# Kernel tuning notes

Hardware: AMD Instinct MI355X
Metric: run time of the kernel (lower is better)

The kernel has to match this reference:

```python
import jax, jax.numpy as jnp
import numpy as np
from jax import lax

N_CHANNELS = 64
N_FILTERS = 256
N_LAYERS = 9  # residual blocks use dilations 2**1 .. 2**(N_LAYERS-1)


def causal_conv1d(x, w, dilation):
    """Causal dilated conv. x: [B,T,Cin], w: [K,Cin,Cout]."""
    pad = (w.shape[0] - 1) * dilation
    return lax.conv_general_dilated(
        x, w, window_strides=(1,), padding=[(pad, 0)],
        rhs_dilation=(dilation,), dimension_numbers=("NWC", "WIO", "NWC"))


def setup_inputs() -> dict:
    key = jax.random.key(0)
    ks = jax.random.split(key, 12)
    B, T, C, F, L = 8, 4096, N_CHANNELS, N_FILTERS, N_LAYERS
    s = lambda fan_in: 1.0 / np.sqrt(fan_in)
    return {
        "x": jax.random.normal(ks[0], (B, T, C), jnp.float32),
        "Wc": jax.random.normal(ks[1], (2, C, F), jnp.float32) * s(2 * C),
        "Wf": jax.random.normal(ks[2], (L - 1, 2, F, F), jnp.float32) * s(2 * F),
        "Wg": jax.random.normal(ks[3], (L - 1, 2, F, F), jnp.float32) * s(2 * F),
        "Wr": jax.random.normal(ks[4], (L - 1, F, F), jnp.float32) * s(F),
        "br": jnp.zeros((L - 1, F), jnp.float32),
        "Ws": jax.random.normal(ks[5], (L - 1, F, F), jnp.float32) * s(F),
        "bs": jnp.zeros((L - 1, F), jnp.float32),
        "Wd1": jax.random.normal(ks[6], (F, C), jnp.float32) * s(F),
        "bd1": jnp.zeros((C,), jnp.float32),
        "Wd2": jax.random.normal(ks[7], (C, C), jnp.float32) * s(C),
        "bd2": jnp.zeros((C,), jnp.float32),
    }


def reference(x, Wc, Wf, Wg, Wr, br, Ws, bs, Wd1, bd1, Wd2, bd2):
    # Initial causal conv, dilation 1, no bias.
    out = causal_conv1d(x, Wc, 1)  # [B,T,F]
    skip_sum = jnp.zeros_like(out)
    for i in range(N_LAYERS - 1):
        d = 2 ** (i + 1)
        f = causal_conv1d(out, Wf[i], d)
        g = causal_conv1d(out, Wg[i], d)
        z = jnp.tanh(f) * jax.nn.sigmoid(g)
        out = out + jnp.einsum("btf,fo->bto", z, Wr[i]) + br[i]
        skip_sum = skip_sum + jnp.einsum("btf,fo->bto", z, Ws[i]) + bs[i]
    h = jax.nn.selu(skip_sum)
    h = jnp.einsum("btf,fc->btc", h, Wd1) + bd1
    h = jax.nn.selu(h)
    h = jnp.einsum("btc,co->bto", h, Wd2) + bd2
    return h
```

## Files before the change

### kernel.cpp

```cpp
#include <hip/hip_runtime.h>
#include <cstdint>

typedef unsigned short u16;
typedef unsigned int u32;
typedef __attribute__((ext_vector_type(8))) short s8v;
typedef __attribute__((ext_vector_type(4))) float f4v;

#define FCH 256

__device__ __forceinline__ float bf2f(u16 u){ return __uint_as_float(((u32)u)<<16); }
__device__ __forceinline__ u16 f2bf(float x){
  u32 u = __float_as_uint(x);
  u += 0x7fffu + ((u>>16)&1u);
  return (u16)(u>>16);
}
__device__ __forceinline__ uint4 pack8(float4 a, float4 b){
  uint4 o;
  o.x = (u32)f2bf(a.x) | ((u32)f2bf(a.y)<<16);
  o.y = (u32)f2bf(a.z) | ((u32)f2bf(a.w)<<16);
  o.z = (u32)f2bf(b.x) | ((u32)f2bf(b.y)<<16);
  o.w = (u32)f2bf(b.z) | ((u32)f2bf(b.w)<<16);
  return o;
}
__device__ __forceinline__ float seluf(float x){
  const float sc = 1.0507009873554805f, al = 1.6732632423543772f;
  return x > 0.f ? sc*x : sc*al*(__expf(x)-1.f);
}
__device__ __forceinline__ s8v ldmask(const u16* p, u32 m){
  uint4 r = *reinterpret_cast<const uint4*>(p);
  r.x &= m; r.y &= m; r.z &= m; r.w &= m;
  s8v v; *reinterpret_cast<uint4*>(&v) = r;
  return v;
}
__device__ __forceinline__ int xcd_tile(int bid, int nT8){
  return nT8 ? ((bid & 7) * nT8 + (bid >> 3)) : bid;
}

__global__ __launch_bounds__(256) void pack_kernel(
    const float* __restrict__ Wc, const float* __restrict__ Wf, const float* __restrict__ Wg,
    const float* __restrict__ Wr, const float* __restrict__ Ws,
    const float* __restrict__ Wd1, const float* __restrict__ Wd2,
    u16* __restrict__ Bp1, u16* __restrict__ Bp2, u16* __restrict__ Bp0,
    u16* __restrict__ BpD1, u16* __restrict__ BpD2)
{
  int gid = blockIdx.x*256 + threadIdx.x;
  int frag = gid >> 6;
  int lane = gid & 63;
  int q = lane >> 4, i15 = lane & 15;
  u16 v[8];
  u16* dst;
  if (frag < 4096) {
    int layer = frag >> 9, rem = frag & 511;
    int kc = rem >> 5, nt = rem & 31;
    int n = nt*16 + i15;
    const float* W = (n < 256) ? Wf : Wg;
    int nn = (n < 256) ? n : n - 256;
    #pragma unroll
    for (int j = 0; j < 8; ++j) {
      int k = kc*32 + q*8 + j;
      int tap = k >> 8, cin = k & 255;
      v[j] = f2bf(W[((size_t)((layer*2 + tap)*256 + cin))*256 + nn]);
    }
    dst = Bp1 + (size_t)frag*512 + lane*8;
  } else if (frag < 6144) {
    int f = frag - 4096;
    int layer = f >> 8, rem = f & 255;
    int kc = rem >> 5, nt = rem & 31;
    int n = nt*16 + i15;
    const float* W = (n < 256) ? Wr : Ws;
    int nn = (n < 256) ? n : n - 256;
    #pragma unroll
    for (int j = 0; j < 8; ++j) {
      int k = kc*32 + q*8 + j;
      v[j] = f2bf(W[((size_t)(layer*256 + k))*256 + nn]);
    }
    dst = Bp2 + (size_t)f*512 + lane*8;
  } else if (frag < 6208) {
    int f = frag - 6144;
    int kc = f >> 4, nt = f & 15;
    int n = nt*16 + i15;
    #pragma unroll
    for (int j = 0; j < 8; ++j) {
      int k = kc*32 + q*8 + j;
      int tap = k >> 6, cin = k & 63;
      v[j] = f2bf(Wc[(size_t)(tap*64 + cin)*256 + n]);
    }
    dst = Bp0 + (size_t)f*512 + lane*8;
  } else if (frag < 6240) {
    int f = frag - 6208;
    int kc = f >> 2, nt = f & 3;
    int n = nt*16 + i15;
    #pragma unroll
    for (int j = 0; j < 8; ++j) {
      int k = kc*32 + q*8 + j;
      v[j] = f2bf(Wd1[(size_t)k*64 + n]);
    }
    dst = BpD1 + (size_t)f*512 + lane*8;
  } else if (frag < 6248) {
    int f = frag - 6240;
    int kc = f >> 2, nt = f & 3;
    int n = nt*16 + i15;
    #pragma unroll
    for (int j = 0; j < 8; ++j) {
      int k = kc*32 + q*8 + j;
      v[j] = f2bf(Wd2[(size_t)k*64 + n]);
    }
    dst = BpD2 + (size_t)f*512 + lane*8;
  } else return;
  uint4 o;
  o.x = (u32)v[0] | ((u32)v[1] << 16);
  o.y = (u32)v[2] | ((u32)v[3] << 16);
  o.z = (u32)v[4] | ((u32)v[5] << 16);
  o.w = (u32)v[6] | ((u32)v[7] << 16);
  *reinterpret_cast<uint4*>(dst) = o;
}

__global__ __launch_bounds__(256, 2) void conv0_kernel(
    const float* __restrict__ x, u16* __restrict__ outBf,
    const u16* __restrict__ Bp0, int nT8)
{
  __shared__ __align__(16) u16 ldsA[2][2048];
  const int tid = threadIdx.x;
  const int w = tid >> 6, lane = tid & 63, q = lane >> 4, i15 = lane & 15;
  const int rb = xcd_tile(blockIdx.x, nT8) * 64;
  const int sm = tid >> 2, sg = tid & 3;
  const int grow = rb + sm;
  const int tpos = grow & 4095;
  const int sunit = ((sm >> 4)*64 + sg*16 + ((sm & 15) ^ (sg << 1))) * 8;
  const int runit = (q*16 + (i15 ^ (q << 1))) * 8;

  f4v acc[4][4];
  #pragma unroll
  for (int jj = 0; jj < 4; ++jj)
    #pragma unroll
    for (int mt = 0; mt < 4; ++mt)
      acc[jj][mt] = (f4v){0.f,0.f,0.f,0.f};

  float4 f0 = {0.f,0.f,0.f,0.f}, f1 = {0.f,0.f,0.f,0.f};
  if (tpos >= 1) {
    const float* px = x + (size_t)(grow-1)*64 + sg*8;
    f0 = *reinterpret_cast<const float4*>(px);
    f1 = *reinterpret_cast<const float4*>(px + 4);
  }
  *reinterpret_cast<uint4*>(&ldsA[0][sunit]) = pack8(f0, f1);
  s8v bcur[4], bnxt[4];
  #pragma unroll
  for (int jj = 0; jj < 4; ++jj)
    bcur[jj] = *reinterpret_cast<const s8v*>(Bp0 + ((size_t)(w + 4*jj)*64 + lane)*8);
  __syncthreads();

  for (int kc = 0; kc < 4; ++kc) {
    const int cur = kc & 1;
    uint4 an = {0u,0u,0u,0u};
    if (kc < 3) {
      int kg = (kc+1)*32 + sg*8;
      int tap = kg >> 6, col = kg & 63;
      float4 g0 = {0.f,0.f,0.f,0.f}, g1 = {0.f,0.f,0.f,0.f};
      if (tap) {
        const float* px = x + (size_t)grow*64 + col;
        g0 = *reinterpret_cast<const float4*>(px);
        g1 = *reinterpret_cast<const float4*>(px + 4);
      } else if (tpos >= 1) {
        const float* px = x + (size_t)(grow-1)*64 + col;
        g0 = *reinterpret_cast<const float4*>(px);
        g1 = *reinterpret_cast<const float4*>(px + 4);
      }
      an = pack8(g0, g1);
      #pragma unroll
      for (int jj = 0; jj < 4; ++jj)
        bnxt[jj] = *reinterpret_cast<const s8v*>(Bp0 + (((size_t)(kc+1)*16 + (w + 4*jj))*64 + lane)*8);
    }
    s8v af[4];
    #pragma unroll
    for (int mt = 0; mt < 4; ++mt)
      af[mt] = *reinterpret_cast<const s8v*>(&ldsA[cur][mt*512 + runit]);
    #pragma unroll
    for (int jj = 0; jj < 4; ++jj)
      #pragma unroll
      for (int mt = 0; mt < 4; ++mt)
        acc[jj][mt] = __builtin_amdgcn_mfma_f32_16x16x32_bf16(af[mt], bcur[jj], acc[jj][mt], 0,0,0);
    if (kc < 3) {
      *reinterpret_cast<uint4*>(&ldsA[cur ^ 1][sunit]) = an;
      #pragma unroll
      for (int jj = 0; jj < 4; ++jj) bcur[jj] = bnxt[jj];
    }
    __syncthreads();
  }

  #pragma unroll
  for (int jj = 0; jj < 4; ++jj) {
    const int cc = (w + 4*jj)*16 + i15;
    #pragma unroll
    for (int mt = 0; mt < 4; ++mt)
      #pragma unroll
      for (int r = 0; r < 4; ++r) {
        const int g2 = rb + mt*16 + q*4 + r;
        outBf[(size_t)g2*FCH + cc] = f2bf(acc[jj][mt][r]);
      }
  }
}

__global__ __launch_bounds__(256, 3) void layer_kernel(
    const u16* __restrict__ inBf, u16* __restrict__ outBf,
    u16* __restrict__ skipB,
    const u16* __restrict__ Bp1, const u16* __restrict__ Bp2,
    const float* __restrict__ br, const float* __restrict__ bs,
    int dil, int first, int nT8)
{
  __shared__ __align__(16) u16 ldsZ[32*264];
  const int tid = threadIdx.x;
  const int w = tid >> 6, lane = tid & 63, q = lane >> 4, i15 = lane & 15;
  const int rb = xcd_tile(blockIdx.x, nT8) * 32;

  f4v acc[8][2];
  #pragma unroll
  for (int jj = 0; jj < 8; ++jj)
    #pragma unroll
    for (int mt = 0; mt < 2; ++mt)
      acc[jj][mt] = (f4v){0.f,0.f,0.f,0.f};

  {
    const u16* a0p[2];
    const u16* a1p[2];
    u32 am[2];
    #pragma unroll
    for (int mt = 0; mt < 2; ++mt) {
      const int row = rb + mt*16 + i15;
      const bool v = (row & 4095) >= dil;
      a0p[mt] = inBf + (size_t)(v ? row - dil : row)*FCH + q*8;
      a1p[mt] = inBf + (size_t)row*FCH + q*8;
      am[mt]  = v ? 0xffffffffu : 0u;
    }

    s8v bb[2][8], aa[2][2];
    #pragma unroll
    for (int jj = 0; jj < 8; ++jj)
      bb[0][jj] = *reinterpret_cast<const s8v*>(Bp1 + ((size_t)(w + 4*jj)*64 + lane)*8);
    #pragma unroll
    for (int mt = 0; mt < 2; ++mt)
      aa[0][mt] = ldmask(a0p[mt], am[mt]);

    #pragma unroll
    for (int kc = 0; kc < 16; ++kc) {
      const int cur = kc & 1, nxt = cur ^ 1;
      if (kc + 1 < 16) {
        const int kn = kc + 1;
        #pragma unroll
        for (int jj = 0; jj < 8; ++jj)
          bb[nxt][jj] = *reinterpret_cast<const s8v*>(Bp1 + (((size_t)kn*32 + (w + 4*jj))*64 + lane)*8);
        if (kn < 8) {
          #pragma unroll
          for (int mt = 0; mt < 2; ++mt)
            aa[nxt][mt] = ldmask(a0p[mt] + kn*32, am[mt]);
        } else {
          #pragma unroll
          for (int mt = 0; mt < 2; ++mt)
            aa[nxt][mt] = *reinterpret_cast<const s8v*>(a1p[mt] + (kn - 8)*32);
        }
      }
      __builtin_amdgcn_s_setprio(1);
      #pragma unroll
      for (int jj = 0; jj < 8; ++jj)
        #pragma unroll
        for (int mt = 0; mt < 2; ++mt)
          acc[jj][mt] = __builtin_amdgcn_mfma_f32_16x16x32_bf16(aa[cur][mt], bb[cur][jj], acc[jj][mt], 0,0,0);
      __builtin_amdgcn_s_setprio(0);
    }
  }

  s8v s2b[2][8];
  #pragma unroll
  for (int jj = 0; jj < 8; ++jj)
    s2b[0][jj] = *reinterpret_cast<const s8v*>(Bp2 + ((size_t)(w + 4*jj)*64 + lane)*8);

  #pragma unroll
  for (int jj = 0; jj < 4; ++jj) {
    const int colb = (w + 4*jj)*16 + i15;
    #pragma unroll
    for (int mt = 0; mt < 2; ++mt)
      #pragma unroll
      for (int r = 0; r < 4; ++r) {
        float f = acc[jj][mt][r];
        float g = acc[jj+4][mt][r];
        float z = (1.f - 2.f/(__expf(2.f*f) + 1.f)) * (1.f/(1.f + __expf(-g)));
        ldsZ[(mt*16 + q*4 + r)*264 + colb] = f2bf(z);
      }
  }
  #pragma unroll
  for (int jj = 0; jj < 8; ++jj)
    #pragma unroll
    for (int mt = 0; mt < 2; ++mt)
      acc[jj][mt] = (f4v){0.f,0.f,0.f,0.f};
  __syncthreads();

  {
    s8v zf[2][2];
    #pragma unroll
    for (int mt = 0; mt < 2; ++mt)
      zf[0][mt] = *reinterpret_cast<const s8v*>(&ldsZ[(mt*16 + i15)*264 + q*8]);
    #pragma unroll
    for (int kc = 0; kc < 8; ++kc) {
      const int cur = kc & 1, nxt = cur ^ 1;
      if (kc + 1 < 8) {
        const int kn = kc + 1;
        #pragma unroll
        for (int jj = 0; jj < 8; ++jj)
          s2b[nxt][jj] = *reinterpret_cast<const s8v*>(Bp2 + (((size_t)kn*32 + (w + 4*jj))*64 + lane)*8);
        #pragma unroll
        for (int mt = 0; mt < 2; ++mt)
          zf[nxt][mt] = *reinterpret_cast<const s8v*>(&ldsZ[(mt*16 + i15)*264 + kn*32 + q*8]);
      }
      __builtin_amdgcn_s_setprio(1);
      #pragma unroll
      for (int jj = 0; jj < 8; ++jj)
        #pragma unroll
        for (int mt = 0; mt < 2; ++mt)
          acc[jj][mt] = __builtin_amdgcn_mfma_f32_16x16x32_bf16(zf[cur][mt], s2b[cur][jj], acc[jj][mt], 0,0,0);
      __builtin_amdgcn_s_setprio(0);
    }
  }

  u16 resv[4][2][4], skv[4][2][4];
  #pragma unroll
  for (int jj = 0; jj < 4; ++jj) {
    const int cc = (w + 4*jj)*16 + i15;
    #pragma unroll
    for (int mt = 0; mt < 2; ++mt)
      #pragma unroll
      for (int r = 0; r < 4; ++r)
        resv[jj][mt][r] = inBf[(size_t)(rb + mt*16 + q*4 + r)*FCH + cc];
  }
  if (!first) {
    #pragma unroll
    for (int jj = 0; jj < 4; ++jj) {
      const int cc = (w + 4*jj)*16 + i15;
      #pragma unroll
      for (int mt = 0; mt < 2; ++mt)
        #pragma unroll
        for (int r = 0; r < 4; ++r)
          skv[jj][mt][r] = skipB[(size_t)(rb + mt*16 + q*4 + r)*FCH + cc];
    }
  }
  #pragma unroll
  for (int jj = 0; jj < 8; ++jj) {
    const int nt = w + 4*jj;
    const bool isR = (jj < 4);
    const int cc = (isR ? nt*16 : (nt-16)*16) + i15;
    const float bias = isR ? br[cc] : bs[cc];
    #pragma unroll
    for (int mt = 0; mt < 2; ++mt)
      #pragma unroll
      for (int r = 0; r < 4; ++r) {
        const int g2 = rb + mt*16 + q*4 + r;
        float vv = acc[jj][mt][r] + bias;
        if (isR) vv += bf2f(resv[jj][mt][r]);
        else if (!first) vv += bf2f(skv[jj-4][mt][r]);
        u16 hv = f2bf(vv);
        if (isR) outBf[(size_t)g2*FCH + cc] = hv;
        else     skipB[(size_t)g2*FCH + cc] = hv;
      }
  }
}

__global__ __launch_bounds__(256, 2) void final_kernel(
    const u16* __restrict__ skipB, const u16* __restrict__ BpD1, const u16* __restrict__ BpD2,
    const float* __restrict__ bd1, const float* __restrict__ bd2, float* __restrict__ outp,
    int nT8)
{
  __shared__ __align__(16) u16 ldsH[64*264];
  __shared__ __align__(16) u16 ldsH2[64*72];
  const int tid = threadIdx.x;
  const int w = tid >> 6, lane = tid & 63, q = lane >> 4, i15 = lane & 15;
  const int rb = xcd_tile(blockIdx.x, nT8) * 64;
  const int sm = tid >> 2, sseg = tid & 3;

  {
    const u16* sp = skipB + (size_t)(rb + sm)*256 + sseg*64;
    u16* dr = &ldsH[sm*264 + sseg*64];
    #pragma unroll
    for (int u = 0; u < 8; ++u) {
      uint4 raw = *reinterpret_cast<const uint4*>(sp + u*8);
      u32 rr[4] = {raw.x, raw.y, raw.z, raw.w};
      uint4 o;
      u32 oo[4];
      #pragma unroll
      for (int p = 0; p < 4; ++p) {
        float e0 = seluf(bf2f((u16)(rr[p] & 0xffffu)));
        float e1 = seluf(bf2f((u16)(rr[p] >> 16)));
        oo[p] = (u32)f2bf(e0) | ((u32)f2bf(e1) << 16);
      }
      o.x = oo[0]; o.y = oo[1]; o.z = oo[2]; o.w = oo[3];
      *reinterpret_cast<uint4*>(dr + u*8) = o;
    }
  }
  __syncthreads();

  f4v a1[4];
  #pragma unroll
  for (int mt = 0; mt < 4; ++mt) a1[mt] = (f4v){0.f,0.f,0.f,0.f};
  for (int kc = 0; kc < 8; ++kc) {
    s8v b = *reinterpret_cast<const s8v*>(BpD1 + ((size_t)(kc*4 + w)*64 + lane)*8);
    #pragma unroll
    for (int mt = 0; mt < 4; ++mt) {
      s8v af = *reinterpret_cast<const s8v*>(&ldsH[(mt*16 + i15)*264 + kc*32 + q*8]);
      a1[mt] = __builtin_amdgcn_mfma_f32_16x16x32_bf16(af, b, a1[mt], 0,0,0);
    }
  }
  const float bb1 = bd1[w*16 + i15];
  #pragma unroll
  for (int mt = 0; mt < 4; ++mt)
    #pragma unroll
    for (int r = 0; r < 4; ++r)
      ldsH2[(mt*16 + q*4 + r)*72 + w*16 + i15] = f2bf(seluf(a1[mt][r] + bb1));
  __syncthreads();

  f4v a2[4];
  #pragma unroll
  for (int mt = 0; mt < 4; ++mt) a2[mt] = (f4v){0.f,0.f,0.f,0.f};
  #pragma unroll
  for (int kc = 0; kc < 2; ++kc) {
    s8v b = *reinterpret_cast<const s8v*>(BpD2 + ((size_t)(kc*4 + w)*64 + lane)*8);
    #pragma unroll
    for (int mt = 0; mt < 4; ++mt) {
      s8v af = *reinterpret_cast<const s8v*>(&ldsH2[(mt*16 + i15)*72 + kc*32 + q*8]);
      a2[mt] = __builtin_amdgcn_mfma_f32_16x16x32_bf16(af, b, a2[mt], 0,0,0);
    }
  }
  const float bb2 = bd2[w*16 + i15];
  #pragma unroll
  for (int mt = 0; mt < 4; ++mt)
    #pragma unroll
    for (int r = 0; r < 4; ++r)
      outp[(size_t)(rb + mt*16 + q*4 + r)*64 + w*16 + i15] = a2[mt][r] + bb2;
}

__global__ __launch_bounds__(256) void zero_kernel(uint4* __restrict__ outp, int n16)
{
  int i = blockIdx.x*256 + threadIdx.x;
  if (i < n16) outp[i] = (uint4){0u,0u,0u,0u};
}

extern "C" void kernel_launch(void* const* d_in, const int* in_sizes, int n_in,
                              void* d_out, int out_size, void* d_ws, size_t ws_size,
                              hipStream_t stream)
{
  (void)n_in;
  const float* x   = (const float*)d_in[0];
  const float* Wc  = (const float*)d_in[1];
  const float* Wf  = (const float*)d_in[2];
  const float* Wg  = (const float*)d_in[3];
  const float* Wr  = (const float*)d_in[4];
  const float* br  = (const float*)d_in[5];
  const float* Ws  = (const float*)d_in[6];
  const float* bs  = (const float*)d_in[7];
  const float* Wd1 = (const float*)d_in[8];
  const float* bd1 = (const float*)d_in[9];
  const float* Wd2 = (const float*)d_in[10];
  const float* bd2 = (const float*)d_in[11];

  const size_t ROWS = (size_t)in_sizes[0] / 64;
  const int gridC = (int)(ROWS / 64);
  const int gridL = (int)(ROWS / 32);
  const int nT8C = (gridC % 8 == 0) ? gridC / 8 : 0;
  const int nT8L = (gridL % 8 == 0) ? gridL / 8 : 0;

  const size_t packsB = (size_t)6248 * 512 * 2;
  const size_t bfBuf  = ROWS * 256 * 2;
  const size_t needB = packsB + 3*bfBuf;

  if (ws_size < needB) {
    int n16 = (out_size * 4) / 16;
    zero_kernel<<<(n16 + 255)/256, 256, 0, stream>>>((uint4*)d_out, n16);
    return;
  }

  char* ws = (char*)d_ws;
  u16* Bp1    = (u16*)ws;            ws += (size_t)4096*512*2;
  u16* Bp2    = (u16*)ws;            ws += (size_t)2048*512*2;
  u16* Bp0    = (u16*)ws;            ws += (size_t)64*512*2;
  u16* BpD1   = (u16*)ws;            ws += (size_t)32*512*2;
  u16* BpD2   = (u16*)ws;            ws += (size_t)8*512*2;
  u16* skipB  = (u16*)ws;            ws += bfBuf;
  u16* bufA   = (u16*)ws;            ws += bfBuf;
  u16* bufB   = (u16*)ws;            ws += bfBuf;

  pack_kernel<<<1562, 256, 0, stream>>>(Wc, Wf, Wg, Wr, Ws, Wd1, Wd2,
                                        Bp1, Bp2, Bp0, BpD1, BpD2);
  conv0_kernel<<<gridC, 256, 0, stream>>>(x, bufA, Bp0, nT8C);
  u16* bufs[2] = {bufA, bufB};
  for (int i = 0; i < 8; ++i) {
    layer_kernel<<<gridL, 256, 0, stream>>>(
        bufs[i & 1], bufs[(i + 1) & 1], skipB,
        Bp1 + (size_t)i*262144, Bp2 + (size_t)i*131072,
        br + i*256, bs + i*256, 2 << i, (i == 0) ? 1 : 0, nT8L);
  }
  final_kernel<<<gridC, 256, 0, stream>>>(skipB, BpD1, BpD2, bd1, bd2,
                                          (float*)d_out, nT8C);
}
```

Before: 492.2 us.

## Switch layer kernel to 32x32x16 bf16 MFMA with repacked weight fragments

The residual-layer kernel now uses 32x32x16 bf16 MFMA instructions in place of 16x16x32. Each wave covers a full 32-row tile with four 32-column accumulators instead of a 2x8 grid of 16x16 tiles. The weight packing for the dilated-conv and residual/skip matrices is changed to match the 32-wide fragment layout, and the epilogue row mapping is rewritten for the 32x32 output layout. This is meant to raise MFMA throughput per instruction and cut the number of A-fragment loads, at the cost of twice as many K-steps and a different register and LDS access pattern.

```diff
diff --git a/kernel.cpp b/kernel.cpp
--- a/kernel.cpp
+++ b/kernel.cpp
@@ -5,6 +5,7 @@
 typedef unsigned int u32;
 typedef __attribute__((ext_vector_type(8))) short s8v;
 typedef __attribute__((ext_vector_type(4))) float f4v;
+typedef __attribute__((ext_vector_type(16))) float f16v;
 
 #define FCH 256
 
@@ -47,17 +48,18 @@
   int frag = gid >> 6;
   int lane = gid & 63;
   int q = lane >> 4, i15 = lane & 15;
+  int hi = lane >> 5, c31 = lane & 31;
   u16 v[8];
   u16* dst;
   if (frag < 4096) {
     int layer = frag >> 9, rem = frag & 511;
-    int kc = rem >> 5, nt = rem & 31;
-    int n = nt*16 + i15;
+    int kc = rem >> 4, nt = rem & 15;
+    int n = nt*32 + c31;
     const float* W = (n < 256) ? Wf : Wg;
     int nn = (n < 256) ? n : n - 256;
     #pragma unroll
     for (int j = 0; j < 8; ++j) {
-      int k = kc*32 + q*8 + j;
+      int k = kc*16 + hi*8 + j;
       int tap = k >> 8, cin = k & 255;
       v[j] = f2bf(W[((size_t)((layer*2 + tap)*256 + cin))*256 + nn]);
     }
@@ -65,13 +67,13 @@
   } else if (frag < 6144) {
     int f = frag - 4096;
     int layer = f >> 8, rem = f & 255;
-    int kc = rem >> 5, nt = rem & 31;
-    int n = nt*16 + i15;
+    int kc = rem >> 4, nt = rem & 15;
+    int n = nt*32 + c31;
     const float* W = (n < 256) ? Wr : Ws;
     int nn = (n < 256) ? n : n - 256;
     #pragma unroll
     for (int j = 0; j < 8; ++j) {
-      int k = kc*32 + q*8 + j;
+      int k = kc*16 + hi*8 + j;
       v[j] = f2bf(W[((size_t)(layer*256 + k))*256 + nn]);
     }
     dst = Bp2 + (size_t)f*512 + lane*8;
@@ -209,156 +211,136 @@
 {
   __shared__ __align__(16) u16 ldsZ[32*264];
   const int tid = threadIdx.x;
-  const int w = tid >> 6, lane = tid & 63, q = lane >> 4, i15 = lane & 15;
+  const int w = tid >> 6, lane = tid & 63, hi = lane >> 5, c31 = lane & 31;
   const int rb = xcd_tile(blockIdx.x, nT8) * 32;
 
-  f4v acc[8][2];
-  #pragma unroll
-  for (int jj = 0; jj < 8; ++jj)
-    #pragma unroll
-    for (int mt = 0; mt < 2; ++mt)
-      acc[jj][mt] = (f4v){0.f,0.f,0.f,0.f};
+  f16v acc[4];
+  #pragma unroll
+  for (int jj = 0; jj < 4; ++jj)
+    #pragma unroll
+    for (int r = 0; r < 16; ++r) acc[jj][r] = 0.f;
 
   {
-    const u16* a0p[2];
-    const u16* a1p[2];
-    u32 am[2];
-    #pragma unroll
-    for (int mt = 0; mt < 2; ++mt) {
-      const int row = rb + mt*16 + i15;
-      const bool v = (row & 4095) >= dil;
-      a0p[mt] = inBf + (size_t)(v ? row - dil : row)*FCH + q*8;
-      a1p[mt] = inBf + (size_t)row*FCH + q*8;
-      am[mt]  = v ? 0xffffffffu : 0u;
-    }
-
-    s8v bb[2][8], aa[2][2];
-    #pragma unroll
-    for (int jj = 0; jj < 8; ++jj)
-      bb[0][jj] = *reinterpret_cast<const s8v*>(Bp1 + ((size_t)(w + 4*jj)*64 + lane)*8);
-    #pragma unroll
-    for (int mt = 0; mt < 2; ++mt)
-      aa[0][mt] = ldmask(a0p[mt], am[mt]);
-
+    const int row = rb + c31;
+    const bool v = (row & 4095) >= dil;
+    const u16* a0 = inBf + (size_t)(v ? row - dil : row)*FCH + hi*8;
+    const u16* a1 = inBf + (size_t)row*FCH + hi*8;
+    const u32 am = v ? 0xffffffffu : 0u;
+
+    s8v bb[2][4], aa[2];
+    #pragma unroll
+    for (int jj = 0; jj < 4; ++jj) {
+      const int nt = (jj < 2) ? (2*w + jj) : (8 + 2*w + (jj - 2));
+      bb[0][jj] = *reinterpret_cast<const s8v*>(Bp1 + ((size_t)nt*64 + lane)*8);
+    }
+    aa[0] = ldmask(a0, am);
+
+    #pragma unroll
+    for (int kc = 0; kc < 32; ++kc) {
+      const int cur = kc & 1, nxt = cur ^ 1;
+      if (kc + 1 < 32) {
+        const int kn = kc + 1;
+        #pragma unroll
+        for (int jj = 0; jj < 4; ++jj) {
+          const int nt = (jj < 2) ? (2*w + jj) : (8 + 2*w + (jj - 2));
+          bb[nxt][jj] = *reinterpret_cast<const s8v*>(Bp1 + (((size_t)kn*16 + nt)*64 + lane)*8);
+        }
+        if (kn < 16) aa[nxt] = ldmask(a0 + kn*16, am);
+        else         aa[nxt] = *reinterpret_cast<const s8v*>(a1 + (kn - 16)*16);
+      }
+      __builtin_amdgcn_s_setprio(1);
+      #pragma unroll
+      for (int jj = 0; jj < 4; ++jj)
+        acc[jj] = __builtin_amdgcn_mfma_f32_32x32x16_bf16(aa[cur], bb[cur][jj], acc[jj], 0,0,0);
+      __builtin_amdgcn_s_setprio(0);
+    }
+  }
+
+  s8v s2b[2][4];
+  #pragma unroll
+  for (int jj = 0; jj < 4; ++jj) {
+    const int nt = (jj < 2) ? (2*w + jj) : (8 + 2*w + (jj - 2));
+    s2b[0][jj] = *reinterpret_cast<const s8v*>(Bp2 + ((size_t)nt*64 + lane)*8);
+  }
+
+  #pragma unroll
+  for (int jj = 0; jj < 2; ++jj) {
+    const int colb = (2*w + jj)*32 + c31;
+    #pragma unroll
+    for (int r = 0; r < 16; ++r) {
+      const int rowid = (r & 3) + 8*(r >> 2) + 4*hi;
+      float f = acc[jj][r];
+      float g = acc[jj+2][r];
+      float z = (1.f - 2.f/(__expf(2.f*f) + 1.f)) * (1.f/(1.f + __expf(-g)));
+      ldsZ[rowid*264 + colb] = f2bf(z);
+    }
+  }
+  #pragma unroll
+  for (int jj = 0; jj < 4; ++jj)
+    #pragma unroll
+    for (int r = 0; r < 16; ++r) acc[jj][r] = 0.f;
+  __syncthreads();
+
+  {
+    s8v zf[2];
+    zf[0] = *reinterpret_cast<const s8v*>(&ldsZ[c31*264 + hi*8]);
     #pragma unroll
     for (int kc = 0; kc < 16; ++kc) {
       const int cur = kc & 1, nxt = cur ^ 1;
       if (kc + 1 < 16) {
         const int kn = kc + 1;
         #pragma unroll
-        for (int jj = 0; jj < 8; ++jj)
-          bb[nxt][jj] = *reinterpret_cast<const s8v*>(Bp1 + (((size_t)kn*32 + (w + 4*jj))*64 + lane)*8);
-        if (kn < 8) {
-          #pragma unroll
-          for (int mt = 0; mt < 2; ++mt)
-            aa[nxt][mt] = ldmask(a0p[mt] + kn*32, am[mt]);
-        } else {
-          #pragma unroll
-          for (int mt = 0; mt < 2; ++mt)
-            aa[nxt][mt] = *reinterpret_cast<const s8v*>(a1p[mt] + (kn - 8)*32);
+        for (int jj = 0; jj < 4; ++jj) {
+          const int nt = (jj < 2) ? (2*w + jj) : (8 + 2*w + (jj - 2));
+          s2b[nxt][jj] = *reinterpret_cast<const s8v*>(Bp2 + (((size_t)kn*16 + nt)*64 + lane)*8);
         }
+        zf[nxt] = *reinterpret_cast<const s8v*>(&ldsZ[c31*264 + kn*16 + hi*8]);
       }
       __builtin_amdgcn_s_setprio(1);
       #pragma unroll
-      for (int jj = 0; jj < 8; ++jj)
-        #pragma unroll
-        for (int mt = 0; mt < 2; ++mt)
-          acc[jj][mt] = __builtin_amdgcn_mfma_f32_16x16x32_bf16(aa[cur][mt], bb[cur][jj], acc[jj][mt], 0,0,0);
+      for (int jj = 0; jj < 4; ++jj)
+        acc[jj] = __builtin_amdgcn_mfma_f32_32x32x16_bf16(zf[cur], s2b[cur][jj], acc[jj], 0,0,0);
       __builtin_amdgcn_s_setprio(0);
     }
   }
 
-  s8v s2b[2][8];
-  #pragma unroll
-  for (int jj = 0; jj < 8; ++jj)
-    s2b[0][jj] = *reinterpret_cast<const s8v*>(Bp2 + ((size_t)(w + 4*jj)*64 + lane)*8);
-
+  u16 resv[2][16], skv[2][16];
+  #pragma unroll
+  for (int jj = 0; jj < 2; ++jj) {
+    const int cc = (2*w + jj)*32 + c31;
+    #pragma unroll
+    for (int r = 0; r < 16; ++r) {
+      const int rowid = (r & 3) + 8*(r >> 2) + 4*hi;
+      resv[jj][r] = inBf[(size_t)(rb + rowid)*FCH + cc];
+    }
+  }
+  if (!first) {
+    #pragma unroll
+    for (int jj = 0; jj < 2; ++jj) {
+      const int cc = (2*w + jj)*32 + c31;
+      #pragma unroll
+      for (int r = 0; r < 16; ++r) {
+        const int rowid = (r & 3) + 8*(r >> 2) + 4*hi;
+        skv[jj][r] = skipB[(size_t)(rb + rowid)*FCH + cc];
+      }
+    }
+  }
   #pragma unroll
   for (int jj = 0; jj < 4; ++jj) {
-    const int colb = (w + 4*jj)*16 + i15;
-    #pragma unroll
-    for (int mt = 0; mt < 2; ++mt)
-      #pragma unroll
-      for (int r = 0; r < 4; ++r) {
-        float f = acc[jj][mt][r];
-        float g = acc[jj+4][mt][r];
-        float z = (1.f - 2.f/(__expf(2.f*f) + 1.f)) * (1.f/(1.f + __expf(-g)));
-        ldsZ[(mt*16 + q*4 + r)*264 + colb] = f2bf(z);
-      }
-  }
-  #pragma unroll
-  for (int jj = 0; jj < 8; ++jj)
-    #pragma unroll
-    for (int mt = 0; mt < 2; ++mt)
-      acc[jj][mt] = (f4v){0.f,0.f,0.f,0.f};
-  __syncthreads();
-
-  {
-    s8v zf[2][2];
-    #pragma unroll
-    for (int mt = 0; mt < 2; ++mt)
-      zf[0][mt] = *reinterpret_cast<const s8v*>(&ldsZ[(mt*16 + i15)*264 + q*8]);
-    #pragma unroll
-    for (int kc = 0; kc < 8; ++kc) {
-      const int cur = kc & 1, nxt = cur ^ 1;
-      if (kc + 1 < 8) {
-        const int kn = kc + 1;
-        #pragma unroll
-        for (int jj = 0; jj < 8; ++jj)
-          s2b[nxt][jj] = *reinterpret_cast<const s8v*>(Bp2 + (((size_t)kn*32 + (w + 4*jj))*64 + lane)*8);
-        #pragma unroll
-        for (int mt = 0; mt < 2; ++mt)
-          zf[nxt][mt] = *reinterpret_cast<const s8v*>(&ldsZ[(mt*16 + i15)*264 + kn*32 + q*8]);
-      }
-      __builtin_amdgcn_s_setprio(1);
-      #pragma unroll
-      for (int jj = 0; jj < 8; ++jj)
-        #pragma unroll
-        for (int mt = 0; mt < 2; ++mt)
-          acc[jj][mt] = __builtin_amdgcn_mfma_f32_16x16x32_bf16(zf[cur][mt], s2b[cur][jj], acc[jj][mt], 0,0,0);
-      __builtin_amdgcn_s_setprio(0);
-    }
-  }
-
-  u16 resv[4][2][4], skv[4][2][4];
-  #pragma unroll
-  for (int jj = 0; jj < 4; ++jj) {
-    const int cc = (w + 4*jj)*16 + i15;
-    #pragma unroll
-    for (int mt = 0; mt < 2; ++mt)
-      #pragma unroll
-      for (int r = 0; r < 4; ++r)
-        resv[jj][mt][r] = inBf[(size_t)(rb + mt*16 + q*4 + r)*FCH + cc];
-  }
-  if (!first) {
-    #pragma unroll
-    for (int jj = 0; jj < 4; ++jj) {
-      const int cc = (w + 4*jj)*16 + i15;
-      #pragma unroll
-      for (int mt = 0; mt < 2; ++mt)
-        #pragma unroll
-        for (int r = 0; r < 4; ++r)
-          skv[jj][mt][r] = skipB[(size_t)(rb + mt*16 + q*4 + r)*FCH + cc];
-    }
-  }
-  #pragma unroll
-  for (int jj = 0; jj < 8; ++jj) {
-    const int nt = w + 4*jj;
-    const bool isR = (jj < 4);
-    const int cc = (isR ? nt*16 : (nt-16)*16) + i15;
+    const bool isR = (jj < 2);
+    const int cc = (2*w + (isR ? jj : jj - 2))*32 + c31;
     const float bias = isR ? br[cc] : bs[cc];
     #pragma unroll
-    for (int mt = 0; mt < 2; ++mt)
-      #pragma unroll
-      for (int r = 0; r < 4; ++r) {
-        const int g2 = rb + mt*16 + q*4 + r;
-        float vv = acc[jj][mt][r] + bias;
-        if (isR) vv += bf2f(resv[jj][mt][r]);
-        else if (!first) vv += bf2f(skv[jj-4][mt][r]);
-        u16 hv = f2bf(vv);
-        if (isR) outBf[(size_t)g2*FCH + cc] = hv;
-        else     skipB[(size_t)g2*FCH + cc] = hv;
-      }
+    for (int r = 0; r < 16; ++r) {
+      const int rowid = (r & 3) + 8*(r >> 2) + 4*hi;
+      const int g2 = rb + rowid;
+      float vv = acc[jj][r] + bias;
+      if (isR) vv += bf2f(resv[jj][r]);
+      else if (!first) vv += bf2f(skv[jj-2][r]);
+      u16 hv = f2bf(vv);
+      if (isR) outBf[(size_t)g2*FCH + cc] = hv;
+      else     skipB[(size_t)g2*FCH + cc] = hv;
+    }
   }
 }
 
```

After: 582.6 us. +18.4%, slower.
